# Kernel tuning notes

Hardware: AMD Instinct MI355X
Metric: run time of the kernel (lower is better)

The kernel has to match this reference:

```python
import jax, jax.numpy as jnp
import numpy as np

B, N, D_M, H, D_K, R, GRID = 2, 2048, 128, 8, 16, 4, 64


def setup_inputs() -> dict:
    key = jax.random.key(0)
    ks = jax.random.split(key, 12)
    z = jax.random.normal(ks[0], (B, N, D_M), dtype=jnp.float32)
    patch_token = jax.random.normal(ks[1], (B, 1, D_M), dtype=jnp.float32)
    positions = jax.random.randint(ks[2], (B, N, 2), 0, GRID, dtype=jnp.int32)
    alive_mask = (jax.random.uniform(ks[3], (B, N, 1)) > 0.1).astype(jnp.float32)
    s = 0.02
    Wq = jax.random.normal(ks[4], (D_M, H * D_K), dtype=jnp.float32) * s
    Wk = jax.random.normal(ks[5], (D_M, H * D_K), dtype=jnp.float32) * s
    Wv = jax.random.normal(ks[6], (D_M, H * D_K), dtype=jnp.float32) * s
    Wo = jax.random.normal(ks[7], (H * D_K, D_M), dtype=jnp.float32) * s
    bq = jnp.zeros((H * D_K,), jnp.float32)
    bk = jnp.zeros((H * D_K,), jnp.float32)
    bv = jnp.zeros((H * D_K,), jnp.float32)
    bo = jnp.zeros((D_M,), jnp.float32)
    rel_bias = jax.random.normal(ks[8], (H, 2 * R + 1, 2 * R + 1), dtype=jnp.float32) * s
    return {"z": z, "patch_token": patch_token, "positions": positions, "alive_mask": alive_mask,
            "Wq": Wq, "bq": bq, "Wk": Wk, "bk": bk, "Wv": Wv, "bv": bv, "Wo": Wo, "bo": bo,
            "rel_bias": rel_bias}


def reference(z, patch_token, positions, alive_mask, Wq, bq, Wk, bk, Wv, bv, Wo, bo, rel_bias):
    B_, N_, _ = z.shape
    H_ = rel_bias.shape[0]
    R_ = (rel_bias.shape[1] - 1) // 2
    dk = Wq.shape[1] // H_
    alive = alive_mask                                   # [B,N,1] float 0/1
    z_a = z * alive
    tokens = jnp.concatenate([z_a, patch_token], axis=1)  # [B,N+1,d_m]
    q = (z_a @ Wq + bq).reshape(B_, N_, H_, dk).transpose(0, 2, 1, 3)       # [B,H,N,dk]
    k = (tokens @ Wk + bk).reshape(B_, N_ + 1, H_, dk).transpose(0, 2, 1, 3)
    v = (tokens @ Wv + bv).reshape(B_, N_ + 1, H_, dk).transpose(0, 2, 1, 3)
    q = q * alive[:, None]                               # [B,1,N,1] broadcast
    logits = jnp.einsum('bhnd,bhmd->bhnm', q, k) / jnp.sqrt(jnp.float32(dk))  # [B,H,N,N+1]
    # Chebyshev mask (delta = pos_i - pos_j)
    delta = positions[:, :, None, :] - positions[:, None, :, :]               # [B,N,N,2]
    cheb = jnp.maximum(jnp.abs(delta[..., 0]), jnp.abs(delta[..., 1]))
    alive_j = alive[:, :, 0] > 0
    not_self = ~jnp.eye(N_, dtype=bool)
    allowed = (cheb <= R_) & alive_j[:, None, :] & not_self[None]
    mask_agents = jnp.where(allowed, 0.0, -1e9).astype(jnp.float32)           # [B,N,N]
    # Relative-position bias (torch uses delta_rel = pos_j - pos_i = -delta)
    dx = -delta[..., 0] + R_
    dy = -delta[..., 1] + R_
    valid = (dx >= 0) & (dx <= 2 * R_) & (dy >= 0) & (dy <= 2 * R_)
    flat = jnp.clip(dx, 0, 2 * R_) * (2 * R_ + 1) + jnp.clip(dy, 0, 2 * R_)   # [B,N,N] int
    table = rel_bias.reshape(H_, -1)
    rel = jnp.moveaxis(jnp.take(table, flat, axis=1), 0, 1)                   # [B,H,N,N]
    rel = rel * valid[:, None].astype(jnp.float32)
    add = mask_agents[:, None] + rel                                          # [B,H,N,N]
    logits = logits + jnp.pad(add, ((0, 0), (0, 0), (0, 0), (0, 1)))          # patch col: mask 0, no bias
    logits = jnp.where(alive[:, None] > 0, logits, -1e9)                      # dead queries
    attn = jax.nn.softmax(logits, axis=-1)
    out = jnp.einsum('bhnm,bhmd->bhnd', attn, v)
    out = out.transpose(0, 2, 1, 3).reshape(B_, N_, H_ * dk)
    out = (out @ Wo + bo) * alive
    return out
```

## Files before the change

### kernel.cpp

```cpp
#include <hip/hip_runtime.h>
#include <math.h>

#define BB 2
#define NN 2048
#define NP1 2049
#define DM 128
#define NH 8
#define DK 16
#define RWIN 4
#define GRID_W 64
#define QPB 8
#define CAND_PQ 160


#define QKV_ROWS 8

__global__ __launch_bounds__(384) void qkv_kernel(
    const float* __restrict__ z, const float* __restrict__ patch,
    const float* __restrict__ Wq, const float* __restrict__ bq,
    const float* __restrict__ Wk, const float* __restrict__ bk,
    const float* __restrict__ Wv, const float* __restrict__ bv,
    float* __restrict__ q, float* __restrict__ k, float* __restrict__ v) {
    __shared__ float zrow[QKV_ROWS][DM];
    const int tid = threadIdx.x;
    const int mat = tid >> 7;
    const int rem = tid & 127;
    const int cg = rem & 31;
    const int rs = rem >> 5;
    const int r0 = blockIdx.x * QKV_ROWS;
    const int NROWS = BB * NP1;

    if (tid < QKV_ROWS * DM / 4) {
        int r = tid >> 5, q4 = tid & 31;
        int row = r0 + r;
        float4 val = make_float4(0.f, 0.f, 0.f, 0.f);
        if (row < NROWS) {
            int b = row / NP1, ti = row % NP1;
            const float* src = (ti < NN) ? (z + ((size_t)b * NN + ti) * DM)
                                         : (patch + (size_t)b * DM);
            val = ((const float4*)src)[q4];
        }
        *((float4*)&zrow[r][q4 * 4]) = val;
    }
    __syncthreads();

    const float* W    = (mat == 0) ? Wq : (mat == 1) ? Wk : Wv;
    const float* bias = (mat == 0) ? bq : (mat == 1) ? bk : bv;

    float a0x = 0.f, a0y = 0.f, a0z = 0.f, a0w = 0.f;
    float a1x = 0.f, a1y = 0.f, a1z = 0.f, a1w = 0.f;
#pragma unroll 8
    for (int kk = 0; kk < DM; ++kk) {
        float4 w4 = *((const float4*)(W + kk * DM + cg * 4));
        float z0 = zrow[rs][kk];
        float z1 = zrow[rs + 4][kk];
        a0x = fmaf(z0, w4.x, a0x); a0y = fmaf(z0, w4.y, a0y);
        a0z = fmaf(z0, w4.z, a0z); a0w = fmaf(z0, w4.w, a0w);
        a1x = fmaf(z1, w4.x, a1x); a1y = fmaf(z1, w4.y, a1y);
        a1z = fmaf(z1, w4.z, a1z); a1w = fmaf(z1, w4.w, a1w);
    }
    float4 b4 = *((const float4*)(bias + cg * 4));
    float4 o0 = make_float4(a0x + b4.x, a0y + b4.y, a0z + b4.z, a0w + b4.w);
    float4 o1 = make_float4(a1x + b4.x, a1y + b4.y, a1z + b4.z, a1w + b4.w);

#pragma unroll
    for (int rr = 0; rr < 2; ++rr) {
        int row = r0 + rs + rr * 4;
        if (row >= NROWS) break;
        float4 val = rr ? o1 : o0;
        int b = row / NP1, ti = row % NP1;
        if (mat == 0) {
            if (ti < NN) ((float4*)(q + ((size_t)b * NN + ti) * DM))[cg] = val;
        } else if (mat == 1) {
            ((float4*)(k + ((size_t)b * NP1 + ti) * DM))[cg] = val;
        } else {
            ((float4*)(v + ((size_t)b * NP1 + ti) * DM))[cg] = val;
        }
    }
}


__global__ __launch_bounds__(256) void attn_out_kernel(
    const float* __restrict__ q, const float* __restrict__ k, const float* __restrict__ v,
    const int* __restrict__ positions, const float* __restrict__ alive,
    const float* __restrict__ rel_bias, const float* __restrict__ Wo,
    const float* __restrict__ bo, float* __restrict__ out) {
    const int tid = threadIdx.x;
    const int qq = tid >> 5;
    const int lane = tid & 31;
    const int h = lane >> 2;
    const int s = lane & 3;
    const int r0 = blockIdx.x * QPB;
    const int b = r0 >> 11;
    const int bi = r0 + qq;

    __shared__ float sbias[NH * 81];
    __shared__ int   spx[QPB], spy[QPB];
    __shared__ float sal[QPB];
    __shared__ int   mcount[QPB];
    __shared__ int   cand[QPB][CAND_PQ];
    __shared__ float po[QPB * 4][DM + 1];
    __shared__ float pl[QPB * 4][NH + 1];
    __shared__ float srow[QPB][DM + 1];

    if (tid < QPB) {
        mcount[tid] = 0;
        int gbi = r0 + tid;
        spx[tid] = positions[gbi * 2 + 0];
        spy[tid] = positions[gbi * 2 + 1];
        sal[tid] = alive[gbi];
    }
    for (int t = tid; t < NH * 81; t += 256) sbias[t] = rel_bias[t];

    const float* kb = k + (size_t)b * NP1 * DM;
    const float* vb = v + (size_t)b * NP1 * DM;

    const float4* qr = (const float4*)(q + (size_t)bi * DM + h * DK);
    float4 q0 = qr[0], q1 = qr[1], q2 = qr[2], q3 = qr[3];
    q0.x *= 0.25f; q0.y *= 0.25f; q0.z *= 0.25f; q0.w *= 0.25f;
    q1.x *= 0.25f; q1.y *= 0.25f; q1.z *= 0.25f; q1.w *= 0.25f;
    q2.x *= 0.25f; q2.y *= 0.25f; q2.z *= 0.25f; q2.w *= 0.25f;
    q3.x *= 0.25f; q3.y *= 0.25f; q3.z *= 0.25f; q3.w *= 0.25f;

    __syncthreads();

    int qx[QPB], qy[QPB], qi[QPB];
    float qa[QPB];
#pragma unroll
    for (int u = 0; u < QPB; ++u) {
        qx[u] = spx[u]; qy[u] = spy[u]; qa[u] = sal[u];
        qi[u] = (r0 + u) & (NN - 1);
    }

    const int2* pb = (const int2*)(positions + (size_t)b * NN * 2);
    const float* ab = alive + (size_t)b * NN;
#pragma unroll
    for (int u = 0; u < NN / 256; ++u) {
        int j = u * 256 + tid;
        int2 pj = pb[j];
        float aj = ab[j];
        if (aj > 0.5f) {
            int packed = j | (pj.x << 16) | (pj.y << 24);
#pragma unroll
            for (int qn = 0; qn < QPB; ++qn) {
                int dx = pj.x - qx[qn]; dx = dx < 0 ? -dx : dx;
                int dy = pj.y - qy[qn]; dy = dy < 0 ? -dy : dy;
                int ch = dx > dy ? dx : dy;
                if (ch <= RWIN && j != qi[qn] && qa[qn] > 0.5f) {
                    int slot = atomicAdd(&mcount[qn], 1);
                    if (slot < CAND_PQ) cand[qn][slot] = packed;
                }
            }
        }
    }
    __syncthreads();
    int M = mcount[qq]; if (M > CAND_PQ) M = CAND_PQ;
    const int pix = qx[qq], piy = qy[qq];

    float l = 0.f;
    float o[16];
#pragma unroll
    for (int d2 = 0; d2 < 16; ++d2) o[d2] = 0.f;

    if (s == 0) {
        const float4* kr = (const float4*)(kb + (size_t)NN * DM + h * DK);
        float4 k0 = kr[0], k1 = kr[1], k2 = kr[2], k3 = kr[3];
        float d0 = q0.x * k0.x; d0 = fmaf(q0.y, k0.y, d0); d0 = fmaf(q0.z, k0.z, d0); d0 = fmaf(q0.w, k0.w, d0);
        float d1 = q1.x * k1.x; d1 = fmaf(q1.y, k1.y, d1); d1 = fmaf(q1.z, k1.z, d1); d1 = fmaf(q1.w, k1.w, d1);
        float d2_ = q2.x * k2.x; d2_ = fmaf(q2.y, k2.y, d2_); d2_ = fmaf(q2.z, k2.z, d2_); d2_ = fmaf(q2.w, k2.w, d2_);
        float d3 = q3.x * k3.x; d3 = fmaf(q3.y, k3.y, d3); d3 = fmaf(q3.z, k3.z, d3); d3 = fmaf(q3.w, k3.w, d3);
        float p = __expf((d0 + d1) + (d2_ + d3));
        const float4* vr = (const float4*)(vb + (size_t)NN * DM + h * DK);
        float4 v0 = vr[0], v1 = vr[1], v2 = vr[2], v3 = vr[3];
        l += p;
        o[0] = fmaf(p, v0.x, o[0]);  o[1] = fmaf(p, v0.y, o[1]);
        o[2] = fmaf(p, v0.z, o[2]);  o[3] = fmaf(p, v0.w, o[3]);
        o[4] = fmaf(p, v1.x, o[4]);  o[5] = fmaf(p, v1.y, o[5]);
        o[6] = fmaf(p, v1.z, o[6]);  o[7] = fmaf(p, v1.w, o[7]);
        o[8] = fmaf(p, v2.x, o[8]);  o[9] = fmaf(p, v2.y, o[9]);
        o[10] = fmaf(p, v2.z, o[10]); o[11] = fmaf(p, v2.w, o[11]);
        o[12] = fmaf(p, v3.x, o[12]); o[13] = fmaf(p, v3.y, o[13]);
        o[14] = fmaf(p, v3.z, o[14]); o[15] = fmaf(p, v3.w, o[15]);
    }

    for (int t = s; t < M; t += 4) {
        int packed = cand[qq][t];
        int j = packed & 0xFFFF;
        const float4* kr = (const float4*)(kb + (size_t)j * DM + h * DK);
        float4 k0 = kr[0], k1 = kr[1], k2 = kr[2], k3 = kr[3];
        const float4* vr = (const float4*)(vb + (size_t)j * DM + h * DK);
        float4 v0 = vr[0], v1 = vr[1], v2 = vr[2], v3 = vr[3];
        float d0 = q0.x * k0.x; d0 = fmaf(q0.y, k0.y, d0); d0 = fmaf(q0.z, k0.z, d0); d0 = fmaf(q0.w, k0.w, d0);
        float d1 = q1.x * k1.x; d1 = fmaf(q1.y, k1.y, d1); d1 = fmaf(q1.z, k1.z, d1); d1 = fmaf(q1.w, k1.w, d1);
        float d2_ = q2.x * k2.x; d2_ = fmaf(q2.y, k2.y, d2_); d2_ = fmaf(q2.z, k2.z, d2_); d2_ = fmaf(q2.w, k2.w, d2_);
        float d3 = q3.x * k3.x; d3 = fmaf(q3.y, k3.y, d3); d3 = fmaf(q3.z, k3.z, d3); d3 = fmaf(q3.w, k3.w, d3);
        int pjx = (packed >> 16) & 0xFF;
        int pjy = (packed >> 24) & 0xFF;
        float bias = sbias[h * 81 + (pjx - pix + RWIN) * 9 + (pjy - piy + RWIN)];
        float p = __expf((d0 + d1) + (d2_ + d3) + bias);
        l += p;
        o[0] = fmaf(p, v0.x, o[0]);  o[1] = fmaf(p, v0.y, o[1]);
        o[2] = fmaf(p, v0.z, o[2]);  o[3] = fmaf(p, v0.w, o[3]);
        o[4] = fmaf(p, v1.x, o[4]);  o[5] = fmaf(p, v1.y, o[5]);
        o[6] = fmaf(p, v1.z, o[6]);  o[7] = fmaf(p, v1.w, o[7]);
        o[8] = fmaf(p, v2.x, o[8]);  o[9] = fmaf(p, v2.y, o[9]);
        o[10] = fmaf(p, v2.z, o[10]); o[11] = fmaf(p, v2.w, o[11]);
        o[12] = fmaf(p, v3.x, o[12]); o[13] = fmaf(p, v3.y, o[13]);
        o[14] = fmaf(p, v3.z, o[14]); o[15] = fmaf(p, v3.w, o[15]);
    }

    {
        const int prow = qq * 4 + s;
#pragma unroll
        for (int d2 = 0; d2 < 16; ++d2) po[prow][h * DK + d2] = o[d2];
        pl[prow][h] = l;
    }
    __syncthreads();
    {
        const int c = tid & 127;
        const int g = tid >> 7;
        const int ch = c >> 4;
#pragma unroll
        for (int qn = 0; qn < 4; ++qn) {
            int qq2 = g * 4 + qn;
            float acc = 0.f, lh = 0.f;
#pragma unroll
            for (int ss = 0; ss < 4; ++ss) {
                acc += po[qq2 * 4 + ss][c];
                lh  += pl[qq2 * 4 + ss][ch];
            }
            srow[qq2][c] = acc / lh;
        }
    }
    __syncthreads();

    {
        const int oq = tid >> 5;
        const int c4 = lane;
        float ax = 0.f, ay = 0.f, az = 0.f, aw = 0.f;
#pragma unroll 8
        for (int kk = 0; kk < DM; ++kk) {
            float sv = srow[oq][kk];
            float4 w4 = *((const float4*)(Wo + kk * DM + c4 * 4));
            ax = fmaf(sv, w4.x, ax); ay = fmaf(sv, w4.y, ay);
            az = fmaf(sv, w4.z, az); aw = fmaf(sv, w4.w, aw);
        }
        float ga = sal[oq] > 0.5f ? 1.f : 0.f;
        float4 b4 = *((const float4*)(bo + c4 * 4));
        float4 r;
        r.x = (ax + b4.x) * ga; r.y = (ay + b4.y) * ga;
        r.z = (az + b4.z) * ga; r.w = (aw + b4.w) * ga;
        ((float4*)(out + (size_t)(r0 + oq) * DM))[c4] = r;
    }
}

extern "C" void kernel_launch(void* const* d_in, const int* in_sizes, int n_in,
                              void* d_out, int out_size, void* d_ws, size_t ws_size,
                              hipStream_t stream) {
    const float* z         = (const float*)d_in[0];
    const float* patch     = (const float*)d_in[1];
    const int*   positions = (const int*)d_in[2];
    const float* alive     = (const float*)d_in[3];
    const float* Wq        = (const float*)d_in[4];
    const float* bq        = (const float*)d_in[5];
    const float* Wk        = (const float*)d_in[6];
    const float* bk        = (const float*)d_in[7];
    const float* Wv        = (const float*)d_in[8];
    const float* bv        = (const float*)d_in[9];
    const float* Wo        = (const float*)d_in[10];
    const float* bo        = (const float*)d_in[11];
    const float* rel_bias  = (const float*)d_in[12];
    float* out = (float*)d_out;

    char* ws = (char*)d_ws;
    size_t off = 0;
    auto alloc = [&](size_t bytes) -> void* {
        void* p = ws + off;
        off += (bytes + 255) & ~(size_t)255;
        return p;
    };
    float* q = (float*)alloc((size_t)BB * NN * DM * 4);
    float* k = (float*)alloc((size_t)BB * NP1 * DM * 4);
    float* v = (float*)alloc((size_t)BB * NP1 * DM * 4);

    qkv_kernel<<<(BB * NP1 + QKV_ROWS - 1) / QKV_ROWS, 384, 0, stream>>>(z, patch, Wq, bq, Wk, bk, Wv, bv, q, k, v);
    attn_out_kernel<<<(BB * NN) / QPB, 256, 0, stream>>>(q, k, v, positions, alive, rel_bias, Wo, bo, out);
}
```

Before: 134.1 us.

## Map one wavefront per query and replace block syncs with wave shuffles

The attention kernel now gives each 64-lane wavefront a single query, with 8 lanes per head, instead of packing 8 queries into a 256-thread block. The candidate scan, the partial-sum reduction and the Wo projection stay inside the wave, using shuffles and wave barriers instead of block-wide __syncthreads and large shared staging buffers. This is meant to cut synchronisation and shared-memory traffic and to raise occupancy. The cost is that each wave rescans all 2048 positions on its own, so position and alive loads grow about eightfold. Every wave also reloads the bias table.

```diff
diff --git a/kernel.cpp b/kernel.cpp
--- a/kernel.cpp
+++ b/kernel.cpp
@@ -9,8 +9,8 @@
 #define DK 16
 #define RWIN 4
 #define GRID_W 64
-#define QPB 8
-#define CAND_PQ 160
+#define WPB 4
+#define CAND 160
 
 
 #define QKV_ROWS 8
@@ -86,32 +86,25 @@
     const float* __restrict__ rel_bias, const float* __restrict__ Wo,
     const float* __restrict__ bo, float* __restrict__ out) {
     const int tid = threadIdx.x;
-    const int qq = tid >> 5;
-    const int lane = tid & 31;
-    const int h = lane >> 2;
-    const int s = lane & 3;
-    const int r0 = blockIdx.x * QPB;
-    const int b = r0 >> 11;
-    const int bi = r0 + qq;
+    const int w = tid >> 6;
+    const int ln = tid & 63;
+    const int h = ln >> 3;
+    const int s = ln & 7;
+    const int bi = blockIdx.x * WPB + w;
+    const int b = bi >> 11;
+    const int i = bi & (NN - 1);
 
     __shared__ float sbias[NH * 81];
-    __shared__ int   spx[QPB], spy[QPB];
-    __shared__ float sal[QPB];
-    __shared__ int   mcount[QPB];
-    __shared__ int   cand[QPB][CAND_PQ];
-    __shared__ float po[QPB * 4][DM + 1];
-    __shared__ float pl[QPB * 4][NH + 1];
-    __shared__ float srow[QPB][DM + 1];
-
-    if (tid < QPB) {
-        mcount[tid] = 0;
-        int gbi = r0 + tid;
-        spx[tid] = positions[gbi * 2 + 0];
-        spy[tid] = positions[gbi * 2 + 1];
-        sal[tid] = alive[gbi];
-    }
-    for (int t = tid; t < NH * 81; t += 256) sbias[t] = rel_bias[t];
-
+    __shared__ int   cand[WPB][CAND];
+    __shared__ int   mcount[WPB];
+    __shared__ float srow[WPB][DM];
+
+    for (int t = ln; t < NH * 81; t += 64) sbias[t] = rel_bias[t];
+    if (ln == 0) mcount[w] = 0;
+
+    const int pix = positions[bi * 2 + 0];
+    const int piy = positions[bi * 2 + 1];
+    const float al = alive[bi];
     const float* kb = k + (size_t)b * NP1 * DM;
     const float* vb = v + (size_t)b * NP1 * DM;
 
@@ -122,40 +115,26 @@
     q2.x *= 0.25f; q2.y *= 0.25f; q2.z *= 0.25f; q2.w *= 0.25f;
     q3.x *= 0.25f; q3.y *= 0.25f; q3.z *= 0.25f; q3.w *= 0.25f;
 
-    __syncthreads();
-
-    int qx[QPB], qy[QPB], qi[QPB];
-    float qa[QPB];
-#pragma unroll
-    for (int u = 0; u < QPB; ++u) {
-        qx[u] = spx[u]; qy[u] = spy[u]; qa[u] = sal[u];
-        qi[u] = (r0 + u) & (NN - 1);
-    }
-
-    const int2* pb = (const int2*)(positions + (size_t)b * NN * 2);
-    const float* ab = alive + (size_t)b * NN;
-#pragma unroll
-    for (int u = 0; u < NN / 256; ++u) {
-        int j = u * 256 + tid;
-        int2 pj = pb[j];
-        float aj = ab[j];
-        if (aj > 0.5f) {
-            int packed = j | (pj.x << 16) | (pj.y << 24);
-#pragma unroll
-            for (int qn = 0; qn < QPB; ++qn) {
-                int dx = pj.x - qx[qn]; dx = dx < 0 ? -dx : dx;
-                int dy = pj.y - qy[qn]; dy = dy < 0 ? -dy : dy;
-                int ch = dx > dy ? dx : dy;
-                if (ch <= RWIN && j != qi[qn] && qa[qn] > 0.5f) {
-                    int slot = atomicAdd(&mcount[qn], 1);
-                    if (slot < CAND_PQ) cand[qn][slot] = packed;
-                }
+    if (al > 0.5f) {
+        const int2* pb = (const int2*)(positions + (size_t)b * NN * 2);
+        const float* ab = alive + (size_t)b * NN;
+#pragma unroll 8
+        for (int u = 0; u < NN / 64; ++u) {
+            int j = u * 64 + ln;
+            int2 pj = pb[j];
+            float aj = ab[j];
+            int dx = pj.x - pix; dx = dx < 0 ? -dx : dx;
+            int dy = pj.y - piy; dy = dy < 0 ? -dy : dy;
+            int ch = dx > dy ? dx : dy;
+            if (ch <= RWIN && aj > 0.5f && j != i) {
+                int slot = atomicAdd(&mcount[w], 1);
+                if (slot < CAND) cand[w][slot] = j | (pj.x << 16) | (pj.y << 24);
             }
         }
     }
-    __syncthreads();
-    int M = mcount[qq]; if (M > CAND_PQ) M = CAND_PQ;
-    const int pix = qx[qq], piy = qy[qq];
+    __builtin_amdgcn_wave_barrier();
+    int M = (al > 0.5f) ? mcount[w] : 0;
+    if (M > CAND) M = CAND;
 
     float l = 0.f;
     float o[16];
@@ -183,8 +162,8 @@
         o[14] = fmaf(p, v3.z, o[14]); o[15] = fmaf(p, v3.w, o[15]);
     }
 
-    for (int t = s; t < M; t += 4) {
-        int packed = cand[qq][t];
+    for (int t = s; t < M; t += 8) {
+        int packed = cand[w][t];
         int j = packed & 0xFFFF;
         const float4* kr = (const float4*)(kb + (size_t)j * DM + h * DK);
         float4 k0 = kr[0], k1 = kr[1], k2 = kr[2], k3 = kr[3];
@@ -209,48 +188,42 @@
         o[14] = fmaf(p, v3.z, o[14]); o[15] = fmaf(p, v3.w, o[15]);
     }
 
+#pragma unroll
+    for (int d = 1; d < 8; d <<= 1) {
+        l += __shfl_xor(l, d, 64);
+#pragma unroll
+        for (int e = 0; e < 16; ++e) o[e] += __shfl_xor(o[e], d, 64);
+    }
+    float rl = 1.f / l;
+    if (s < 4) {
+#pragma unroll
+        for (int e = 0; e < 4; ++e) srow[w][h * DK + s * 4 + e] = o[s * 4 + e] * rl;
+    }
+    __builtin_amdgcn_wave_barrier();
+
     {
-        const int prow = qq * 4 + s;
-#pragma unroll
-        for (int d2 = 0; d2 < 16; ++d2) po[prow][h * DK + d2] = o[d2];
-        pl[prow][h] = l;
-    }
-    __syncthreads();
-    {
-        const int c = tid & 127;
-        const int g = tid >> 7;
-        const int ch = c >> 4;
-#pragma unroll
-        for (int qn = 0; qn < 4; ++qn) {
-            int qq2 = g * 4 + qn;
-            float acc = 0.f, lh = 0.f;
-#pragma unroll
-            for (int ss = 0; ss < 4; ++ss) {
-                acc += po[qq2 * 4 + ss][c];
-                lh  += pl[qq2 * 4 + ss][ch];
-            }
-            srow[qq2][c] = acc / lh;
-        }
-    }
-    __syncthreads();
-
-    {
-        const int oq = tid >> 5;
-        const int c4 = lane;
+        const int m = ln >> 1;
+        const int half = ln & 1;
+        const float* Wb = Wo + (size_t)half * 64 * DM + m * 4;
+        const float* sr = &srow[w][half * 64];
         float ax = 0.f, ay = 0.f, az = 0.f, aw = 0.f;
-#pragma unroll 8
-        for (int kk = 0; kk < DM; ++kk) {
-            float sv = srow[oq][kk];
-            float4 w4 = *((const float4*)(Wo + kk * DM + c4 * 4));
+#pragma unroll 16
+        for (int kk = 0; kk < 64; ++kk) {
+            float sv = sr[kk];
+            float4 w4 = *((const float4*)(Wb + (size_t)kk * DM));
             ax = fmaf(sv, w4.x, ax); ay = fmaf(sv, w4.y, ay);
             az = fmaf(sv, w4.z, az); aw = fmaf(sv, w4.w, aw);
         }
-        float ga = sal[oq] > 0.5f ? 1.f : 0.f;
-        float4 b4 = *((const float4*)(bo + c4 * 4));
-        float4 r;
-        r.x = (ax + b4.x) * ga; r.y = (ay + b4.y) * ga;
-        r.z = (az + b4.z) * ga; r.w = (aw + b4.w) * ga;
-        ((float4*)(out + (size_t)(r0 + oq) * DM))[c4] = r;
+        ax += __shfl_xor(ax, 1, 64); ay += __shfl_xor(ay, 1, 64);
+        az += __shfl_xor(az, 1, 64); aw += __shfl_xor(aw, 1, 64);
+        if (half == 0) {
+            float ga = al > 0.5f ? 1.f : 0.f;
+            float4 b4 = *((const float4*)(bo + m * 4));
+            float4 r;
+            r.x = (ax + b4.x) * ga; r.y = (ay + b4.y) * ga;
+            r.z = (az + b4.z) * ga; r.w = (aw + b4.w) * ga;
+            ((float4*)(out + (size_t)bi * DM))[m] = r;
+        }
     }
 }
 
@@ -284,5 +257,5 @@
     float* v = (float*)alloc((size_t)BB * NP1 * DM * 4);
 
     qkv_kernel<<<(BB * NP1 + QKV_ROWS - 1) / QKV_ROWS, 384, 0, stream>>>(z, patch, Wq, bq, Wk, bk, Wv, bv, q, k, v);
-    attn_out_kernel<<<(BB * NN) / QPB, 256, 0, stream>>>(q, k, v, positions, alive, rel_bias, Wo, bo, out);
+    attn_out_kernel<<<(BB * NN) / WPB, 256, 0, stream>>>(q, k, v, positions, alive, rel_bias, Wo, bo, out);
 }
```

Result: slower. 144.3 us (+7.6%).
